# Kernel tuning notes

Measured on AMD Instinct MI355X. Metric: run time of the kernel, lower is better.

## Reference

```python
import jax, jax.numpy as jnp
import numpy as np

EMBED = 384
HEADS = 12
DH = EMBED // HEADS  # 32, lucidrains default dim_heads = dim // heads
EPS = 1e-5


def _layernorm(t, g, b):
    mu = jnp.mean(t, axis=-1, keepdims=True)
    var = jnp.mean(jnp.square(t - mu), axis=-1, keepdims=True)
    return (t - mu) * jax.lax.rsqrt(var + EPS) * g + b


def _self_attn(t2, Wq, Wkv, Wo, bo):
    # t2: (N, T, D) -> multi-head self attention (lucidrains SelfAttention)
    N, T, D = t2.shape
    q = t2 @ Wq
    k, v = jnp.split(t2 @ Wkv, 2, axis=-1)
    def split_heads(z):
        return z.reshape(N, T, HEADS, DH).transpose(0, 2, 1, 3)  # (N,H,T,DH)
    q, k, v = map(split_heads, (q, k, v))
    dots = jnp.einsum('nhie,nhje->nhij', q, k) * (DH ** -0.5)
    o = jnp.einsum('nhij,nhje->nhie', jax.nn.softmax(dots, axis=-1), v)
    o = o.transpose(0, 2, 1, 3).reshape(N, T, D)
    return o @ Wo + bo


def _axial(xcl, axis, Wq, Wkv, Wo, bo):
    # xcl channels-last: (b, 3, 16, 16, C); attend along `axis` (1, 2 or 3)
    y = jnp.moveaxis(xcl, axis, -2)
    sh = y.shape
    o = _self_attn(y.reshape(-1, sh[-2], sh[-1]), Wq, Wkv, Wo, bo)
    return jnp.moveaxis(o.reshape(sh), -2, axis)


def setup_inputs() -> dict:
    key = jax.random.key(0)
    ks = jax.random.split(key, 24)
    d, mlp = EMBED, 4 * EMBED
    s = 0.02
    inp = {'x': jax.random.normal(ks[0], (128, 384, 3, 16, 16), jnp.float32)}
    for i in range(3):  # one SelfAttention per axial dim (slice, h, w)
        inp[f'Wq{i}'] = (jax.random.normal(ks[1 + 3 * i], (d, d)) * s).astype(jnp.float32)
        inp[f'Wkv{i}'] = (jax.random.normal(ks[2 + 3 * i], (d, 2 * d)) * s).astype(jnp.float32)
        inp[f'Wo{i}'] = (jax.random.normal(ks[3 + 3 * i], (d, d)) * s).astype(jnp.float32)
        inp[f'bo{i}'] = jnp.zeros((d,), jnp.float32)
    inp['g1'] = jnp.ones((d,), jnp.float32)
    inp['be1'] = jnp.zeros((d,), jnp.float32)
    inp['W1m'] = (jax.random.normal(ks[10], (d, mlp)) * s).astype(jnp.float32)
    inp['b1m'] = jnp.zeros((mlp,), jnp.float32)
    inp['W2m'] = (jax.random.normal(ks[11], (mlp, d)) * s).astype(jnp.float32)
    inp['b2m'] = jnp.zeros((d,), jnp.float32)
    inp['g2'] = jnp.ones((d,), jnp.float32)
    inp['be2'] = jnp.zeros((d,), jnp.float32)
    return inp


def reference(x, Wq0, Wkv0, Wo0, bo0, Wq1, Wkv1, Wo1, bo1, Wq2, Wkv2, Wo2, bo2,
              g1, be1, W1m, b1m, W2m, b2m, g2, be2):
    # x: (B, C=384, 3, 16, 16); dropout is identity in eval mode
    xcl = jnp.moveaxis(x, 1, -1)  # (B, 3, 16, 16, C)
    attn = (_axial(xcl, 1, Wq0, Wkv0, Wo0, bo0)
            + _axial(xcl, 2, Wq1, Wkv1, Wo1, bo1)
            + _axial(xcl, 3, Wq2, Wkv2, Wo2, bo2))  # sum_axial_out=True
    xcl = xcl + attn  # residual
    B = xcl.shape[0]
    t = xcl.reshape(B, 3 * 16 * 16, EMBED)  # == x.flatten(2).transpose(1,2)
    t = _layernorm(t, g1, be1)
    m = jax.nn.gelu(t @ W1m + b1m, approximate=False) @ W2m + b2m
    t = _layernorm(t + m, g2, be2)
    return jnp.moveaxis(t.reshape(B, 3, 16, 16, EMBED), -1, 1)
```

## Files before the change

kernel.cpp:

```cpp
#include <hip/hip_runtime.h>

typedef unsigned short u16;
typedef __bf16 bf16;
typedef bf16  bf16x4 __attribute__((ext_vector_type(4)));
typedef bf16  bf16x8 __attribute__((ext_vector_type(8)));
typedef float f32x4  __attribute__((ext_vector_type(4)));

__device__ __forceinline__ u16  f2b(float v) { return __builtin_bit_cast(u16, (bf16)v); }
__device__ __forceinline__ float b2f(u16 b)  { return (float)__builtin_bit_cast(bf16, b); }

__global__ void probe_dtype(const float* xf, int* flag) {
    __shared__ int cnt[256];
    const int tid = threadIdx.x;
    int good = 0;
#pragma unroll
    for (int i = 0; i < 4; ++i) {
        const float a = fabsf(xf[tid * 4 + i]);
        if (a > 9.5e-7f && a < 1.0e6f) good++;
    }
    cnt[tid] = good;
    __syncthreads();
    if (tid == 0) { int s = 0; for (int i = 0; i < 256; ++i) s += cnt[i]; *flag = (s > 512) ? 1 : 0; }
}

__global__ void cvt_vec(const void* in, bf16* out, int n, const int* flag) {
    const int f32 = *flag;
    for (int i = blockIdx.x * 256 + threadIdx.x; i < n; i += gridDim.x * 256)
        out[i] = f32 ? (bf16)(((const float*)in)[i])
                     : __builtin_bit_cast(bf16, ((const u16*)in)[i]);
}

__global__ void sum3_vec(const void* a, const void* b, const void* c, bf16* out, int n, const int* flag) {
    const int f32 = *flag;
    for (int i = blockIdx.x * 256 + threadIdx.x; i < n; i += gridDim.x * 256) {
        float va, vb, vc;
        if (f32) { va = ((const float*)a)[i]; vb = ((const float*)b)[i]; vc = ((const float*)c)[i]; }
        else { va = b2f(((const u16*)a)[i]); vb = b2f(((const u16*)b)[i]); vc = b2f(((const u16*)c)[i]); }
        out[i] = (bf16)(va + vb + vc);
    }
}

__global__ void transpose_cvt(const void* in, u16* out, size_t base_off, int R, int C, int ostride, const int* flag) {
    __shared__ u16 tile[32][34];
    const int f32 = *flag;
    const int c0 = blockIdx.x * 32, r0 = blockIdx.y * 32;
    const size_t bi = base_off + (size_t)blockIdx.z * R * C;
    const size_t bo = (size_t)blockIdx.z * C * ostride;
    const int tx = threadIdx.x, ty = threadIdx.y;
#pragma unroll
    for (int i = 0; i < 4; ++i) {
        const size_t idx = bi + (size_t)(r0 + ty + i * 8) * C + c0 + tx;
        tile[ty + i * 8][tx] = f32 ? f2b(((const float*)in)[idx]) : ((const u16*)in)[idx];
    }
    __syncthreads();
#pragma unroll
    for (int i = 0; i < 4; ++i)
        out[bo + (size_t)(c0 + ty + i * 8) * ostride + r0 + tx] = tile[tx][ty + i * 8];
}

__global__ void transpose_out(const u16* in, void* out, size_t base_off, int R, int C, const int* flag) {
    __shared__ u16 tile[32][34];
    const int f32 = *flag;
    const int c0 = blockIdx.x * 32, r0 = blockIdx.y * 32;
    const size_t bi = (size_t)blockIdx.z * R * C;
    const size_t bo = base_off + (size_t)blockIdx.z * R * C;
    const int tx = threadIdx.x, ty = threadIdx.y;
#pragma unroll
    for (int i = 0; i < 4; ++i)
        tile[ty + i * 8][tx] = in[bi + (size_t)(r0 + ty + i * 8) * C + c0 + tx];
    __syncthreads();
#pragma unroll
    for (int i = 0; i < 4; ++i) {
        const size_t o = bo + (size_t)(c0 + ty + i * 8) * R + r0 + tx;
        const u16 v = tile[tx][ty + i * 8];
        if (f32) ((float*)out)[o] = b2f(v); else ((u16*)out)[o] = v;
    }
}

__device__ __forceinline__ void gld_lds16(const bf16* g, bf16* l) {
    __builtin_amdgcn_global_load_lds((__attribute__((address_space(1))) void*)g,
                                     (__attribute__((address_space(3))) void*)l,
                                     16, 0, 0);
}

template<int MODE>
__global__ __launch_bounds__(512)
void gemm256(const bf16* __restrict__ A, const bf16* __restrict__ BT,
             bf16* C, const bf16* __restrict__ bias, int M, int N, int K)
{
    __shared__ __align__(16) bf16 sm[65536];
    const int tid = threadIdx.x;

    const int gx = gridDim.x, gy = gridDim.y;
    int lin = blockIdx.y * gx + blockIdx.x;
    const int nwg = gx * gy;
    const int q = nwg >> 3, r8 = nwg & 7;
    const int xcd = lin & 7, idx = lin >> 3;
    lin = (xcd < r8 ? xcd * (q + 1) : r8 * (q + 1) + (xcd - r8) * q) + idx;
    const int bm0 = (lin / gy) * 256;
    const int bn0 = (lin % gy) * 256;

    const int lane = tid & 63, wid = tid >> 6;
    const int wr = wid >> 2, wc = wid & 3;
    const int fr = lane & 15, fg = lane >> 4;
    const int arow = tid >> 3;
    const int scol = ((tid & 7) ^ (arow & 7)) << 3;

    const bf16* Ab = A  + (size_t)(bm0 + arow) * K + scol;
    const bf16* Bb = BT + (size_t)(bn0 + arow) * K + scol;

    bf16* const lA0 = sm;
    bf16* const lA1 = sm + 16384;
    bf16* const lB0 = sm + 32768;
    bf16* const lB1 = sm + 49152;

    f32x4 acc[8][4] = {};
    const int NT = K >> 6;

#pragma unroll
    for (int i = 0; i < 4; ++i) gld_lds16(Ab + (size_t)i * 64 * K, lA0 + i * 4096 + tid * 8);
#pragma unroll
    for (int i = 0; i < 4; ++i) gld_lds16(Bb + (size_t)i * 64 * K, lB0 + i * 4096 + tid * 8);
    __syncthreads();

    const int sw = fr & 7;
    for (int t = 0; t < NT; ++t) {
        if (t + 1 < NT) {
            const int k0 = (t + 1) << 6;
            bf16* la = ((t + 1) & 1) ? lA1 : lA0;
            bf16* lb = ((t + 1) & 1) ? lB1 : lB0;
#pragma unroll
            for (int i = 0; i < 4; ++i) gld_lds16(Ab + k0 + (size_t)i * 64 * K, la + i * 4096 + tid * 8);
#pragma unroll
            for (int i = 0; i < 4; ++i) gld_lds16(Bb + k0 + (size_t)i * 64 * K, lb + i * 4096 + tid * 8);
        }
        const bf16* la = (t & 1) ? lA1 : lA0;
        const bf16* lb = (t & 1) ? lB1 : lB0;
#pragma unroll
        for (int kk = 0; kk < 2; ++kk) {
            const int so = ((((kk << 2) + fg) ^ sw) << 3);
            bf16x8 bfv[4];
#pragma unroll
            for (int n = 0; n < 4; ++n)
                bfv[n] = *(const bf16x8*)&lb[(wc * 64 + n * 16 + fr) * 64 + so];
#pragma unroll
            for (int m = 0; m < 8; ++m) {
                const bf16x8 af = *(const bf16x8*)&la[(wr * 128 + m * 16 + fr) * 64 + so];
#pragma unroll
                for (int n = 0; n < 4; ++n)
                    acc[m][n] = __builtin_amdgcn_mfma_f32_16x16x32_bf16(af, bfv[n], acc[m][n], 0, 0, 0);
            }
        }
        __syncthreads();
    }

#pragma unroll
    for (int n = 0; n < 4; ++n) {
        const int col = wc * 64 + n * 16 + fr;
        const float bv = (MODE == 2) ? (float)bias[bn0 + col] : 0.f;
#pragma unroll
        for (int m = 0; m < 8; ++m) {
            const int row0 = wr * 128 + m * 16 + fg * 4;
#pragma unroll
            for (int r = 0; r < 4; ++r) {
                float v = acc[m][n][r];
                if (MODE == 2) { v += bv; v = 0.5f * v * (1.f + erff(v * 0.70710678118654752f)); }
                sm[(row0 + r) * 256 + col] = (bf16)v;
            }
        }
    }
    __syncthreads();
#pragma unroll
    for (int it = 0; it < 16; ++it) {
        const int chunk = it * 512 + tid;
        const int row = chunk >> 5, c8 = (chunk & 31) << 3;
        *(bf16x8*)&C[(size_t)(bm0 + row) * N + bn0 + c8] = *(const bf16x8*)&sm[row * 256 + c8];
    }
}

template<int MODE>
__global__ __launch_bounds__(256)
void gemm_bt(const bf16* __restrict__ A, const bf16* __restrict__ BT,
             bf16* C, const bf16* __restrict__ bias,
             const bf16* add, int M, int N, int K)
{
    __shared__ __align__(16) bf16 sm[4][8192];
    const int tid = threadIdx.x;

    const int gx = gridDim.x, gy = gridDim.y;
    int lin = blockIdx.y * gx + blockIdx.x;
    const int nwg = gx * gy;
    const int q = nwg >> 3, r8 = nwg & 7;
    const int xcd = lin & 7, idx = lin >> 3;
    lin = (xcd < r8 ? xcd * (q + 1) : r8 * (q + 1) + (xcd - r8) * q) + idx;
    const int bm0 = (lin / gy) * 128;
    const int bn0 = (lin % gy) * 128;

    const int lane = tid & 63, wid = tid >> 6;
    const int wr = wid >> 1, wc = wid & 1;
    const int fr = lane & 15, fg = lane >> 4;
    const int arow = tid >> 3;
    const int scol = ((tid & 7) ^ (arow & 7)) << 3;

    const bf16* Ab = A  + (size_t)(bm0 + arow) * K + scol;
    const bf16* Bb = BT + (size_t)(bn0 + arow) * K + scol;

    f32x4 acc[4][4] = {};
    const int NT = K >> 6;
    {
        bf16* la = sm[0];
        bf16* lb = sm[1];
#pragma unroll
        for (int i = 0; i < 4; ++i) gld_lds16(Ab + (size_t)i * 32 * K, &la[i * 2048 + tid * 8]);
#pragma unroll
        for (int i = 0; i < 4; ++i) gld_lds16(Bb + (size_t)i * 32 * K, &lb[i * 2048 + tid * 8]);
    }
    __syncthreads();

    const int sw = fr & 7;
    for (int t = 0; t < NT; ++t) {
        if (t + 1 < NT) {
            const int k0 = (t + 1) << 6;
            bf16* la = sm[2 * ((t + 1) & 1)];
            bf16* lb = sm[2 * ((t + 1) & 1) + 1];
#pragma unroll
            for (int i = 0; i < 4; ++i) gld_lds16(Ab + k0 + (size_t)i * 32 * K, &la[i * 2048 + tid * 8]);
#pragma unroll
            for (int i = 0; i < 4; ++i) gld_lds16(Bb + k0 + (size_t)i * 32 * K, &lb[i * 2048 + tid * 8]);
        }
        const bf16* la = sm[2 * (t & 1)];
        const bf16* lb = sm[2 * (t & 1) + 1];
#pragma unroll
        for (int kk = 0; kk < 2; ++kk) {
            bf16x8 af[4], bfv[4];
#pragma unroll
            for (int m = 0; m < 4; ++m)
                af[m] = *(const bf16x8*)&la[(wr * 64 + m * 16 + fr) * 64 + ((((kk << 2) + fg) ^ sw) << 3)];
#pragma unroll
            for (int n = 0; n < 4; ++n)
                bfv[n] = *(const bf16x8*)&lb[(wc * 64 + n * 16 + fr) * 64 + ((((kk << 2) + fg) ^ sw) << 3)];
#pragma unroll
            for (int m = 0; m < 4; ++m)
#pragma unroll
                for (int n = 0; n < 4; ++n)
                    acc[m][n] = __builtin_amdgcn_mfma_f32_16x16x32_bf16(af[m], bfv[n], acc[m][n], 0, 0, 0);
        }
        __syncthreads();
    }

    float* lc = (float*)sm;
#pragma unroll
    for (int n = 0; n < 4; ++n) {
        const int col = wc * 64 + n * 16 + fr;
#pragma unroll
        for (int m = 0; m < 4; ++m) {
            const int row0 = wr * 64 + m * 16 + fg * 4;
#pragma unroll
            for (int r2 = 0; r2 < 4; ++r2)
                lc[(row0 + r2) * 128 + col] = acc[m][n][r2];
        }
    }
    __syncthreads();
    const f32x4* lc4 = (const f32x4*)sm;
#pragma unroll
    for (int i = 0; i < 16; ++i) {
        const int chunk = i * 256 + tid;
        const int row = chunk >> 5, cb = (chunk & 31) * 4;
        const size_t goff = (size_t)(bm0 + row) * N + bn0 + cb;
        const f32x4 v = lc4[chunk];
        bf16x4 o;
        if (MODE == 1) {
            const bf16x4 bv = *(const bf16x4*)&bias[bn0 + cb];
            const bf16x4 av = *(const bf16x4*)&add[goff];
#pragma unroll
            for (int e = 0; e < 4; ++e) o[e] = (bf16)(v[e] + (float)bv[e] + (float)av[e]);
        } else {
#pragma unroll
            for (int e = 0; e < 4; ++e) o[e] = (bf16)v[e];
        }
        *(bf16x4*)&C[goff] = o;
    }
}

__global__ __launch_bounds__(256)
void attn16(const bf16* __restrict__ QKV, bf16* __restrict__ O, int tstride, int lastmul, int qs, int os)
{
    const int lane = threadIdx.x & 63;
    const int gw   = (blockIdx.x * 256 + threadIdx.x) >> 6;
    const int head = gw % 12;
    const int seq  = gw / 12;
    const int b    = seq / 48, r2 = seq % 48;
    const int s    = r2 >> 4, last = r2 & 15;
    const int tbase = b * 768 + s * 256 + last * lastmul;
    const int fr = lane & 15, fg = lane >> 4;

    const size_t rowQ = (size_t)(tbase + fr * tstride) * qs + head * 32 + fg * 8;
    const bf16x8 kf = *(const bf16x8*)(QKV + rowQ + 384);
    const bf16x8 qf = *(const bf16x8*)(QKV + rowQ);
    const f32x4 z = {0.f, 0.f, 0.f, 0.f};
    f32x4 S = __builtin_amdgcn_mfma_f32_16x16x32_bf16(kf, qf, z, 0, 0, 0);

    const float sc = 0.17677669529663687f;
    float mx = fmaxf(fmaxf(S[0], S[1]), fmaxf(S[2], S[3]));
    mx = fmaxf(mx, __shfl_xor(mx, 16));
    mx = fmaxf(mx, __shfl_xor(mx, 32));
    float p[4], sum = 0.f;
#pragma unroll
    for (int r = 0; r < 4; ++r) { p[r] = __expf((S[r] - mx) * sc); sum += p[r]; }
    sum += __shfl_xor(sum, 16);
    sum += __shfl_xor(sum, 32);
    const float inv = 1.f / sum;

    bf16x8 pa;
#pragma unroll
    for (int j = 0; j < 8; ++j) {
        const int srcg = 2 * fg + (j >> 2);
        const float v = __shfl(p[j & 3], fr + 16 * (srcg & 3));
        pa[j] = (bf16)(fg < 2 ? v * inv : 0.f);
    }

#pragma unroll
    for (int t = 0; t < 2; ++t) {
        bf16x8 vf;
#pragma unroll
        for (int j = 0; j < 8; ++j) {
            const int key = fg * 8 + j;
            vf[j] = (fg < 2)
                ? QKV[(size_t)(tbase + key * tstride) * qs + 768 + head * 32 + fr + 16 * t]
                : (bf16)0.f;
        }
        f32x4 o = __builtin_amdgcn_mfma_f32_16x16x32_bf16(pa, vf, z, 0, 0, 0);
#pragma unroll
        for (int r = 0; r < 4; ++r)
            O[(size_t)(tbase + (fg * 4 + r) * tstride) * os + head * 32 + fr + 16 * t] = (bf16)o[r];
    }
}

__global__ __launch_bounds__(256)
void attn3(const bf16* __restrict__ QKV, bf16* __restrict__ O, int qs, int os)
{
    const int t    = blockIdx.x * 256 + threadIdx.x;
    const int head = t % 12;
    const int seq  = t / 12;
    const int b    = seq >> 8, hw = seq & 255;
    const size_t base  = (size_t)(b * 768 + hw) * qs + head * 32;
    const size_t tstep = (size_t)256 * qs;

    float s[3][3] = {};
#pragma unroll
    for (int c = 0; c < 4; ++c) {
        bf16x8 q[3], k[3];
#pragma unroll
        for (int i = 0; i < 3; ++i) {
            q[i] = *(const bf16x8*)(QKV + base + i * tstep + c * 8);
            k[i] = *(const bf16x8*)(QKV + base + i * tstep + 384 + c * 8);
        }
#pragma unroll
        for (int i = 0; i < 3; ++i)
#pragma unroll
            for (int j = 0; j < 3; ++j) {
                float a = 0.f;
#pragma unroll
                for (int e = 0; e < 8; ++e) a += (float)q[i][e] * (float)k[j][e];
                s[i][j] += a;
            }
    }
    const float sc = 0.17677669529663687f;
    float p[3][3];
#pragma unroll
    for (int i = 0; i < 3; ++i) {
        const float mx = fmaxf(s[i][0], fmaxf(s[i][1], s[i][2]));
        float sum = 0.f;
#pragma unroll
        for (int j = 0; j < 3; ++j) { p[i][j] = __expf((s[i][j] - mx) * sc); sum += p[i][j]; }
        const float inv = 1.f / sum;
#pragma unroll
        for (int j = 0; j < 3; ++j) p[i][j] *= inv;
    }
    const size_t obase = (size_t)(b * 768 + hw) * os + head * 32;
#pragma unroll
    for (int c = 0; c < 4; ++c) {
        bf16x8 v[3];
#pragma unroll
        for (int j = 0; j < 3; ++j) v[j] = *(const bf16x8*)(QKV + base + j * tstep + 768 + c * 8);
#pragma unroll
        for (int i = 0; i < 3; ++i) {
            bf16x8 ov;
#pragma unroll
            for (int e = 0; e < 8; ++e)
                ov[e] = (bf16)(p[i][0] * (float)v[0][e] + p[i][1] * (float)v[1][e] + p[i][2] * (float)v[2][e]);
            *(bf16x8*)(O + obase + (size_t)i * 256 * os + c * 8) = ov;
        }
    }
}

__global__ __launch_bounds__(256)
void ln_kernel(const bf16* __restrict__ in, bf16* __restrict__ out,
               const bf16* __restrict__ g, const bf16* __restrict__ be, int ntok)
{
    const int w    = (blockIdx.x * 256 + threadIdx.x) >> 6;
    const int lane = threadIdx.x & 63;
    if (w >= ntok) return;
    const bf16* row = in + (size_t)w * 384;
    float x[6], sum = 0.f;
#pragma unroll
    for (int i = 0; i < 6; ++i) { x[i] = (float)row[lane + i * 64]; sum += x[i]; }
#pragma unroll
    for (int o = 32; o >= 1; o >>= 1) sum += __shfl_xor(sum, o);
    const float mu = sum * (1.f / 384.f);
    float vs = 0.f;
#pragma unroll
    for (int i = 0; i < 6; ++i) { const float d = x[i] - mu; vs += d * d; }
#pragma unroll
    for (int o = 32; o >= 1; o >>= 1) vs += __shfl_xor(vs, o);
    const float rstd = rsqrtf(vs * (1.f / 384.f) + 1e-5f);
    bf16* orow = out + (size_t)w * 384;
#pragma unroll
    for (int i = 0; i < 6; ++i)
        orow[lane + i * 64] = (bf16)((x[i] - mu) * rstd * (float)g[lane + i * 64] + (float)be[lane + i * 64]);
}

extern "C" void kernel_launch(void* const* d_in, const int* in_sizes, int n_in,
                              void* d_out, int out_size, void* d_ws, size_t ws_size,
                              hipStream_t stream)
{
    const void* x = d_in[0];
    const void *Wq[3], *Wkv[3], *Wo[3], *bo[3];
    for (int i = 0; i < 3; ++i) {
        Wq[i]  = d_in[1 + 4 * i];
        Wkv[i] = d_in[2 + 4 * i];
        Wo[i]  = d_in[3 + 4 * i];
        bo[i]  = d_in[4 + 4 * i];
    }
    const void* g1  = d_in[13];
    const void* be1 = d_in[14];
    const void* W1m = d_in[15];
    const void* b1m = d_in[16];
    const void* W2m = d_in[17];
    const void* b2m = d_in[18];
    const void* g2  = d_in[19];
    const void* be2 = d_in[20];

    char* ws = (char*)d_ws;
    bf16* qkvT = (bf16*)(ws);
    bf16* woTf = (bf16*)(ws + 2654208ull);
    bf16* w1mT = (bf16*)(ws + 3538944ull);
    bf16* w2mT = (bf16*)(ws + 4718592ull);
    bf16 *vboS, *vg1, *vbe1, *vg2, *vbe2, *vb1m, *vb2m;
    {
        char* vp = ws + 5898240ull;
        vboS = (bf16*)(vp);
        vg1  = (bf16*)(vp + 768);        vbe1 = (bf16*)(vp + 1536);
        vg2  = (bf16*)(vp + 2304);       vbe2 = (bf16*)(vp + 3072);
        vb1m = (bf16*)(vp + 3840);       vb2m = (bf16*)(vp + 6912);
    }
    int* dflag = (int*)(ws + 5909504ull);
    const size_t WB = 6553600ull;

    int NB = 32;
    while (NB > 2) {
        size_t need = WB + (size_t)NB * 768 * (3 * 384 + 2 * 1152 + 1536) * 2;
        if (need <= ws_size) break;
        NB >>= 1;
    }
    const int Tc = NB * 768;
    const size_t tokB = (size_t)Tc * 384 * 2;
    bf16* Xc    = (bf16*)(ws + WB);
    bf16* ABc   = (bf16*)(ws + WB + tokB);
    bf16* T1c   = (bf16*)(ws + WB + 2 * tokB);
    bf16* ATOc  = (bf16*)(ws + WB + 3 * tokB);
    bf16* QKVc  = (bf16*)(ws + WB + 6 * tokB);
    bf16* BIGc  = (bf16*)(ws + WB + 9 * tokB);

    probe_dtype<<<1, 256, 0, stream>>>((const float*)x, dflag);
    sum3_vec<<<2, 256, 0, stream>>>(bo[0], bo[1], bo[2], vboS, 384, dflag);
    cvt_vec<<<2, 256, 0, stream>>>(g1,  vg1,  384,  dflag);
    cvt_vec<<<2, 256, 0, stream>>>(be1, vbe1, 384,  dflag);
    cvt_vec<<<2, 256, 0, stream>>>(g2,  vg2,  384,  dflag);
    cvt_vec<<<2, 256, 0, stream>>>(be2, vbe2, 384,  dflag);
    cvt_vec<<<6, 256, 0, stream>>>(b1m, vb1m, 1536, dflag);
    cvt_vec<<<2, 256, 0, stream>>>(b2m, vb2m, 384,  dflag);

    const dim3 tb(32, 8);
    for (int i = 0; i < 3; ++i) {
        transpose_cvt<<<dim3(12, 12, 1), tb, 0, stream>>>(Wq[i],  (u16*)(qkvT + (size_t)(i * 1152) * 384),       0, 384, 384, 384, dflag);
        transpose_cvt<<<dim3(24, 12, 1), tb, 0, stream>>>(Wkv[i], (u16*)(qkvT + (size_t)(i * 1152 + 384) * 384), 0, 384, 768, 384, dflag);
        transpose_cvt<<<dim3(12, 12, 1), tb, 0, stream>>>(Wo[i],  (u16*)(woTf + i * 384),                        0, 384, 384, 1152, dflag);
    }
    transpose_cvt<<<dim3(48, 12, 1), tb, 0, stream>>>(W1m, (u16*)w1mT, 0, 384, 1536, 384,  dflag);
    transpose_cvt<<<dim3(12, 48, 1), tb, 0, stream>>>(W2m, (u16*)w2mT, 0, 1536, 384, 1536, dflag);

    for (int b0 = 0; b0 < 128; b0 += NB) {
        const size_t xoff = (size_t)b0 * 384 * 768;
        transpose_cvt<<<dim3(24, 12, NB), tb, 0, stream>>>(x, (u16*)Xc, xoff, 384, 768, 384, dflag);

        for (int i = 0; i < 3; ++i) {
            gemm_bt<0><<<dim3(Tc / 128, 9), 256, 0, stream>>>(Xc, qkvT + (size_t)(i * 1152) * 384,
                                                              QKVc, nullptr, nullptr, Tc, 1152, 384);
            if (i == 0)      attn3 <<<NB * 12,  256, 0, stream>>>(QKVc, ATOc,              1152, 1152);
            else if (i == 1) attn16<<<NB * 144, 256, 0, stream>>>(QKVc, ATOc + 384, 16, 1, 1152, 1152);
            else             attn16<<<NB * 144, 256, 0, stream>>>(QKVc, ATOc + 768, 1, 16, 1152, 1152);
        }

        gemm_bt<1><<<dim3(Tc / 128, 3), 256, 0, stream>>>(ATOc, woTf, ABc, vboS, Xc, Tc, 384, 1152);

        ln_kernel<<<Tc / 4, 256, 0, stream>>>(ABc, T1c, vg1, vbe1, Tc);
        gemm256<2><<<dim3(Tc / 256, 6), 512, 0, stream>>>(T1c, w1mT, BIGc, vb1m, Tc, 1536, 384);
        gemm_bt<1><<<dim3(Tc / 128, 3), 256, 0, stream>>>(BIGc, w2mT, ABc, vb2m, T1c, Tc, 384, 1536);
        ln_kernel<<<Tc / 4, 256, 0, stream>>>(ABc, Xc, vg2, vbe2, Tc);
        transpose_out<<<dim3(12, 24, NB), tb, 0, stream>>>((const u16*)Xc, d_out, xoff, 768, 384, dflag);
    }
}
```

Baseline: 1.558 ms.

## Single-buffer gemm_bt LDS and split epilogue to raise occupancy

Removes double buffering in the bf16 GEMM, halving shared memory from 64KB to 32KB. The fp32 epilogue staging is split into two 64-row halves so it fits the smaller buffer. A launch bound of 5 waves per SIMD is added so more workgroups can be resident per CU, trading overlap of global loads with MFMA inside a block for cross-block latency hiding. The cost is extra barriers per K-step, loads that no longer overlap compute within a block, and possible register pressure.

```diff
diff --git a/kernel.cpp b/kernel.cpp
--- a/kernel.cpp
+++ b/kernel.cpp
@@ -179,12 +179,12 @@
 }
 
 template<int MODE>
-__global__ __launch_bounds__(256)
+__global__ __launch_bounds__(256, 5)
 void gemm_bt(const bf16* __restrict__ A, const bf16* __restrict__ BT,
              bf16* C, const bf16* __restrict__ bias,
              const bf16* add, int M, int N, int K)
 {
-    __shared__ __align__(16) bf16 sm[4][8192];
+    __shared__ __align__(16) bf16 sm[16384];
     const int tid = threadIdx.x;
 
     const int gx = gridDim.x, gy = gridDim.y;
@@ -205,80 +205,73 @@
     const bf16* Ab = A  + (size_t)(bm0 + arow) * K + scol;
     const bf16* Bb = BT + (size_t)(bn0 + arow) * K + scol;
 
+    bf16* const lA = sm;
+    bf16* const lB = sm + 8192;
+
     f32x4 acc[4][4] = {};
     const int NT = K >> 6;
-    {
-        bf16* la = sm[0];
-        bf16* lb = sm[1];
-#pragma unroll
-        for (int i = 0; i < 4; ++i) gld_lds16(Ab + (size_t)i * 32 * K, &la[i * 2048 + tid * 8]);
-#pragma unroll
-        for (int i = 0; i < 4; ++i) gld_lds16(Bb + (size_t)i * 32 * K, &lb[i * 2048 + tid * 8]);
-    }
-    __syncthreads();
-
     const int sw = fr & 7;
+
     for (int t = 0; t < NT; ++t) {
-        if (t + 1 < NT) {
-            const int k0 = (t + 1) << 6;
-            bf16* la = sm[2 * ((t + 1) & 1)];
-            bf16* lb = sm[2 * ((t + 1) & 1) + 1];
-#pragma unroll
-            for (int i = 0; i < 4; ++i) gld_lds16(Ab + k0 + (size_t)i * 32 * K, &la[i * 2048 + tid * 8]);
-#pragma unroll
-            for (int i = 0; i < 4; ++i) gld_lds16(Bb + k0 + (size_t)i * 32 * K, &lb[i * 2048 + tid * 8]);
-        }
-        const bf16* la = sm[2 * (t & 1)];
-        const bf16* lb = sm[2 * (t & 1) + 1];
+        __syncthreads();
+        const int k0 = t << 6;
+#pragma unroll
+        for (int i = 0; i < 4; ++i) gld_lds16(Ab + k0 + (size_t)i * 32 * K, lA + i * 2048 + tid * 8);
+#pragma unroll
+        for (int i = 0; i < 4; ++i) gld_lds16(Bb + k0 + (size_t)i * 32 * K, lB + i * 2048 + tid * 8);
+        __syncthreads();
 #pragma unroll
         for (int kk = 0; kk < 2; ++kk) {
             bf16x8 af[4], bfv[4];
 #pragma unroll
             for (int m = 0; m < 4; ++m)
-                af[m] = *(const bf16x8*)&la[(wr * 64 + m * 16 + fr) * 64 + ((((kk << 2) + fg) ^ sw) << 3)];
+                af[m] = *(const bf16x8*)&lA[(wr * 64 + m * 16 + fr) * 64 + ((((kk << 2) + fg) ^ sw) << 3)];
 #pragma unroll
             for (int n = 0; n < 4; ++n)
-                bfv[n] = *(const bf16x8*)&lb[(wc * 64 + n * 16 + fr) * 64 + ((((kk << 2) + fg) ^ sw) << 3)];
+                bfv[n] = *(const bf16x8*)&lB[(wc * 64 + n * 16 + fr) * 64 + ((((kk << 2) + fg) ^ sw) << 3)];
 #pragma unroll
             for (int m = 0; m < 4; ++m)
 #pragma unroll
                 for (int n = 0; n < 4; ++n)
                     acc[m][n] = __builtin_amdgcn_mfma_f32_16x16x32_bf16(af[m], bfv[n], acc[m][n], 0, 0, 0);
         }
+    }
+    __syncthreads();
+
+    float* lc = (float*)sm;
+#pragma unroll
+    for (int half = 0; half < 2; ++half) {
+        if (wr == half) {
+#pragma unroll
+            for (int n = 0; n < 4; ++n) {
+                const int col = wc * 64 + n * 16 + fr;
+#pragma unroll
+                for (int m = 0; m < 4; ++m)
+#pragma unroll
+                    for (int r2 = 0; r2 < 4; ++r2)
+                        lc[(m * 16 + fg * 4 + r2) * 128 + col] = acc[m][n][r2];
+            }
+        }
         __syncthreads();
-    }
-
-    float* lc = (float*)sm;
-#pragma unroll
-    for (int n = 0; n < 4; ++n) {
-        const int col = wc * 64 + n * 16 + fr;
-#pragma unroll
-        for (int m = 0; m < 4; ++m) {
-            const int row0 = wr * 64 + m * 16 + fg * 4;
-#pragma unroll
-            for (int r2 = 0; r2 < 4; ++r2)
-                lc[(row0 + r2) * 128 + col] = acc[m][n][r2];
-        }
-    }
-    __syncthreads();
-    const f32x4* lc4 = (const f32x4*)sm;
-#pragma unroll
-    for (int i = 0; i < 16; ++i) {
-        const int chunk = i * 256 + tid;
-        const int row = chunk >> 5, cb = (chunk & 31) * 4;
-        const size_t goff = (size_t)(bm0 + row) * N + bn0 + cb;
-        const f32x4 v = lc4[chunk];
-        bf16x4 o;
-        if (MODE == 1) {
-            const bf16x4 bv = *(const bf16x4*)&bias[bn0 + cb];
-            const bf16x4 av = *(const bf16x4*)&add[goff];
-#pragma unroll
-            for (int e = 0; e < 4; ++e) o[e] = (bf16)(v[e] + (float)bv[e] + (float)av[e]);
-        } else {
-#pragma unroll
-            for (int e = 0; e < 4; ++e) o[e] = (bf16)v[e];
-        }
-        *(bf16x4*)&C[goff] = o;
+#pragma unroll
+        for (int i = 0; i < 8; ++i) {
+            const int chunk = i * 256 + tid;
+            const int row = chunk >> 5, cb = (chunk & 31) * 4;
+            const size_t goff = (size_t)(bm0 + half * 64 + row) * N + bn0 + cb;
+            const f32x4 v = ((const f32x4*)lc)[chunk];
+            bf16x4 o;
+            if (MODE == 1) {
+                const bf16x4 bv = *(const bf16x4*)&bias[bn0 + cb];
+                const bf16x4 av = *(const bf16x4*)&add[goff];
+#pragma unroll
+                for (int e = 0; e < 4; ++e) o[e] = (bf16)(v[e] + (float)bv[e] + (float)av[e]);
+            } else {
+#pragma unroll
+                for (int e = 0; e < 4; ++e) o[e] = (bf16)v[e];
+            }
+            *(bf16x4*)&C[goff] = o;
+        }
+        __syncthreads();
     }
 }
 
```

Result: slower. 3.016 ms (+93.6%).
